# Kernel tuning notes

Measured on AMD Instinct MI355X. Metric: run time of the kernel, lower is better.

Reference implementation:

```python
import jax, jax.numpy as jnp
import numpy as np

N, E, CIN, H, HEADS, B = 50000, 800000, 16, 64, 3, 64
D0 = HEADS * H            # conv1 out (heads concatenated) = 192
D1 = D0 + CIN             # x1 dim = 208
D2 = 2 * D1               # x2 dim = 416
MLP_IN = 3 * D2           # 1248
MLP_HID = MLP_IN // 2     # 624
EPS = 1e-5


def setup_inputs() -> dict:
    key = jax.random.key(0)
    ks = jax.random.split(key, 24)
    r = lambda k, s, sc=0.05: (jax.random.normal(k, s, dtype=jnp.float32) * sc)
    inp = {
        'x': jax.random.normal(ks[0], (N, CIN), dtype=jnp.float32),
        'edge_index': jax.random.randint(ks[1], (2, E), 0, N, dtype=jnp.int32),
        'edge_attr': jax.random.normal(ks[2], (E, 4), dtype=jnp.float32),
        'batch': jnp.sort(jax.random.randint(ks[3], (N,), 0, B, dtype=jnp.int32)),
        # conv1 (GeneralConv, heads=3, concat): msg/edge/self linears -> D0
        'W_msg1': r(ks[4], (CIN, D0)), 'b_msg1': jnp.zeros((D0,), jnp.float32),
        'W_edge1': r(ks[5], (4, D0)), 'b_edge1': jnp.zeros((D0,), jnp.float32),
        'W_self1': r(ks[6], (CIN, D0)), 'b_self1': jnp.zeros((D0,), jnp.float32),
        'g1': jnp.ones((D0,), jnp.float32), 'be1': jnp.zeros((D0,), jnp.float32),
        # conv2 (GeneralConv, heads=1, in==out -> identity self)
        'W_msg2': r(ks[7], (D1, D1)), 'b_msg2': jnp.zeros((D1,), jnp.float32),
        'W_edge2': r(ks[8], (4, D1)), 'b_edge2': jnp.zeros((D1,), jnp.float32),
        'g2': jnp.ones((D1,), jnp.float32), 'be2': jnp.zeros((D1,), jnp.float32),
        # MLP head
        'W_l1': r(ks[9], (MLP_IN, MLP_HID)), 'b_l1': jnp.zeros((MLP_HID,), jnp.float32),
        'alpha': jnp.asarray(0.25, jnp.float32),  # PReLU default
        'W_l2': r(ks[10], (MLP_HID, 2)), 'b_l2': jnp.zeros((2,), jnp.float32),
    }
    return inp


def _bn(h, g, b):
    m = h.mean(axis=0)
    v = h.var(axis=0)  # biased, like torch BatchNorm training mode
    return (h - m) * jax.lax.rsqrt(v + EPS) * g + b


def reference(x, edge_index, edge_attr, batch,
              W_msg1, b_msg1, W_edge1, b_edge1, W_self1, b_self1, g1, be1,
              W_msg2, b_msg2, W_edge2, b_edge2, g2, be2,
              W_l1, b_l1, alpha, W_l2, b_l2):
    src, dst = edge_index[0], edge_index[1]
    # conv1: gather -> linear msg + edge feature -> scatter-add -> + self linear
    m1 = x[src] @ W_msg1 + b_msg1 + edge_attr @ W_edge1 + b_edge1   # [E, D0]
    h1 = jax.ops.segment_sum(m1, dst, num_segments=N) + (x @ W_self1 + b_self1)
    h1 = _bn(h1, g1, be1)
    x1 = jnp.concatenate([h1, x], axis=1)                           # [N, D1]
    # conv2 (identity self-connection since in==out)
    m2 = x1[src] @ W_msg2 + b_msg2 + edge_attr @ W_edge2 + b_edge2  # [E, D1]
    h2 = jax.ops.segment_sum(m2, dst, num_segments=N) + x1
    h2 = _bn(h2, g2, be2)
    x2 = jnp.concatenate([h2, x1], axis=1)                          # [N, D2]
    # global add / mean / max pooling by graph id
    s = jax.ops.segment_sum(x2, batch, num_segments=B)
    cnt = jax.ops.segment_sum(jnp.ones((x2.shape[0], 1), x2.dtype), batch, num_segments=B)
    mean = s / jnp.maximum(cnt, 1.0)
    mx = jax.ops.segment_max(x2, batch, num_segments=B)
    pooled = jnp.concatenate([s, mx, mean], axis=1)                 # [B, 3*D2]
    # MLP head: Linear -> Dropout(0) -> PReLU -> Linear -> log_softmax
    h = pooled @ W_l1 + b_l1
    h = jnp.where(h >= 0, h, alpha * h)
    logits = h @ W_l2 + b_l2
    return jax.nn.log_softmax(logits, axis=-1)
```

## Files before the change

### kernel.cpp

```cpp
#include <hip/hip_runtime.h>

typedef __attribute__((ext_vector_type(8))) short short8;
typedef __attribute__((ext_vector_type(4))) float f32x4;
typedef unsigned short u16;
typedef unsigned int u32;

__device__ __forceinline__ u16 f2bf(float f) {
  u32 u = __float_as_uint(f);
  u = (u + 0x7fffu + ((u >> 16) & 1u)) >> 16;
  return (u16)u;
}
__device__ __forceinline__ float bf2f(u16 v) { return __uint_as_float((u32)v << 16); }
__device__ __forceinline__ void atomAddF(float* p, float v) { unsafeAtomicAdd(p, v); }
__device__ __forceinline__ void addp(float* v, u32 p) {
  v[0] += bf2f((u16)p);
  v[1] += bf2f((u16)(p >> 16));
}

__global__ void prep_k(const float* __restrict__ Wm1, const float* __restrict__ We1,
                       const float* __restrict__ Ws1, const float* __restrict__ Wm2,
                       const float* __restrict__ Wl1, const float* __restrict__ x,
                       const int* __restrict__ batch, u16* __restrict__ Wp1,
                       u16* __restrict__ Wp2, u16* __restrict__ Wp3,
                       u16* __restrict__ xbf, int* __restrict__ gstart,
                       int* __restrict__ gend, int* __restrict__ deg,
                       float* __restrict__ bns1p, float* __restrict__ bns2p, int N, int E) {
  int tid = blockIdx.x * 256 + threadIdx.x;
  if (tid < 64 * 192) {
    int k = tid / 192, n = tid % 192;
    float v = 0.f;
    if (k < 16) v = Wm1[k * 192 + n];
    else if (k < 20) v = We1[(k - 16) * 192 + n];
    else if (k < 36) v = Ws1[(k - 20) * 192 + n];
    Wp1[((k >> 3) * 192 + n) * 8 + (k & 7)] = f2bf(v);
  }
  if (tid < 224 * 208) {
    int k = tid / 208, n = tid % 208;
    float v = (k < 208) ? Wm2[k * 208 + n] : 0.f;
    Wp2[((k >> 3) * 208 + n) * 8 + (k & 7)] = f2bf(v);
  }
  if (tid < N * 8) {
    float2 p = *(const float2*)(x + (size_t)tid * 2);
    *(u32*)(xbf + (size_t)tid * 2) = (u32)f2bf(p.x) | ((u32)f2bf(p.y) << 16);
  }
  if (tid < N) {
    int b = batch[tid];
    if (tid == 0 || batch[tid - 1] != b) gstart[b] = tid;
    if (tid == N - 1 || batch[tid + 1] != b) gend[b] = tid;
    deg[tid] = 0;
  }
  if (tid < 64 * 384) bns1p[tid] = 0.f;
  if (tid < 64 * 832) bns2p[tid] = 0.f;
  if (tid < 1248 * 624) {
    int k = tid / 624, n = tid % 624;
    Wp3[((size_t)(k >> 3) * 624 + n) * 8 + (k & 7)] = f2bf(Wl1[(size_t)k * 624 + n]);
  }
}

__global__ void count_k(const int* __restrict__ ei, int* __restrict__ deg,
                        int* __restrict__ ord, int E) {
  int e = blockIdx.x * 256 + threadIdx.x;
  if (e >= E) return;
  ord[e] = atomicAdd(&deg[ei[E + e]], 1);
}

__global__ void scanA_k(const int* __restrict__ deg, int* __restrict__ bsum, int N) {
  __shared__ int sh[256];
  int t = threadIdx.x;
  int i = blockIdx.x * 256 + t;
  sh[t] = (i < N) ? deg[i] : 0;
  __syncthreads();
  for (int off = 128; off > 0; off >>= 1) {
    if (t < off) sh[t] += sh[t + off];
    __syncthreads();
  }
  if (t == 0) bsum[blockIdx.x] = sh[0];
}

__global__ void scanC_k(const int* __restrict__ deg, const int* __restrict__ bsum,
                        int* __restrict__ rowptr, int N, int nb) {
  __shared__ int sb2[256];
  __shared__ int sh[256];
  int t = threadIdx.x;
  int bv = (t < nb) ? bsum[t] : 0;
  sb2[t] = bv;
  __syncthreads();
  for (int off = 1; off < 256; off <<= 1) {
    int u = (t >= off) ? sb2[t - off] : 0;
    __syncthreads();
    sb2[t] += u;
    __syncthreads();
  }
  int bpref = (blockIdx.x == 0) ? 0 : sb2[blockIdx.x - 1];
  int i = blockIdx.x * 256 + t;
  int d = (i < N) ? deg[i] : 0;
  sh[t] = d;
  __syncthreads();
  for (int off = 1; off < 256; off <<= 1) {
    int u = (t >= off) ? sh[t - off] : 0;
    __syncthreads();
    sh[t] += u;
    __syncthreads();
  }
  int excl = sh[t] - d + bpref;
  if (i < N) {
    rowptr[i] = excl;
    if (i == N - 1) rowptr[N] = excl + d;
  }
}

__global__ void scatter_k(const int* __restrict__ ei, const float* __restrict__ ea,
                          const int* __restrict__ ord, const int* __restrict__ rowptr,
                          int4* __restrict__ se16, int E) {
  int e = blockIdx.x * 256 + threadIdx.x;
  if (e >= E) return;
  int s = ei[e], d = ei[E + e];
  float4 w = *(const float4*)(ea + (size_t)e * 4);
  int slot = rowptr[d] + ord[e];
  int4 ent;
  ent.x = s;
  ent.y = (int)((u32)f2bf(w.x) | ((u32)f2bf(w.y) << 16));
  ent.z = (int)((u32)f2bf(w.z) | ((u32)f2bf(w.w) << 16));
  ent.w = 0;
  se16[slot] = ent;
}

__global__ void __launch_bounds__(256) gath1_k(
    const int4* __restrict__ se16, const int* __restrict__ rowptr,
    const u16* __restrict__ xbf, u16* __restrict__ acc1c, int N) {
  int tid = threadIdx.x;
  int nl = tid >> 4, q = tid & 15;
  int n = blockIdx.x * 16 + nl;
  bool nval = n < N;
  int j0 = nval ? rowptr[n] : 0;
  int j1 = nval ? rowptr[n + 1] : 0;
  float v[20];
#pragma unroll
  for (int i = 0; i < 20; ++i) v[i] = 0.f;
  {
    int j = j0 + q;
    bool a0 = j < j1, a1 = (j + 16) < j1;
    int jj0 = a0 ? j : 0;
    int jj1 = a1 ? (j + 16) : 0;
    int4 p0 = se16[jj0];
    int4 p1 = se16[jj1];
    const uint4* xs0 = (const uint4*)(xbf + (size_t)(a0 ? p0.x : 0) * 16);
    uint4 x00 = xs0[0], x01 = xs0[1];
    const uint4* xs1 = (const uint4*)(xbf + (size_t)(a1 ? p1.x : 0) * 16);
    uint4 x10 = xs1[0], x11 = xs1[1];
    if (a0) {
      addp(v + 0, x00.x); addp(v + 2, x00.y); addp(v + 4, x00.z); addp(v + 6, x00.w);
      addp(v + 8, x01.x); addp(v + 10, x01.y); addp(v + 12, x01.z); addp(v + 14, x01.w);
      addp(v + 16, (u32)p0.y); addp(v + 18, (u32)p0.z);
    }
    if (a1) {
      addp(v + 0, x10.x); addp(v + 2, x10.y); addp(v + 4, x10.z); addp(v + 6, x10.w);
      addp(v + 8, x11.x); addp(v + 10, x11.y); addp(v + 12, x11.z); addp(v + 14, x11.w);
      addp(v + 16, (u32)p1.y); addp(v + 18, (u32)p1.z);
    }
    for (j += 32; j < j1; j += 16) {
      int4 p = se16[j];
      const uint4* xs = (const uint4*)(xbf + (size_t)p.x * 16);
      uint4 x0 = xs[0], x1 = xs[1];
      addp(v + 0, x0.x); addp(v + 2, x0.y); addp(v + 4, x0.z); addp(v + 6, x0.w);
      addp(v + 8, x1.x); addp(v + 10, x1.y); addp(v + 12, x1.z); addp(v + 14, x1.w);
      addp(v + 16, (u32)p.y); addp(v + 18, (u32)p.z);
    }
  }
#pragma unroll
  for (int i = 0; i < 20; ++i) {
    v[i] += __shfl_xor(v[i], 1);
    v[i] += __shfl_xor(v[i], 2);
    v[i] += __shfl_xor(v[i], 4);
    v[i] += __shfl_xor(v[i], 8);
  }
  if (nval) {
    float degf = (float)(j1 - j0);
    int t0 = q * 2, t1 = t0 + 1;
    float f0 = (t0 < 20) ? v[t0] : ((t0 == 20) ? degf : 0.f);
    float f1 = (t1 < 20) ? v[t1] : ((t1 == 20) ? degf : 0.f);
    *(u32*)(acc1c + (size_t)n * 32 + q * 2) = (u32)f2bf(f0) | ((u32)f2bf(f1) << 16);
  }
}

__global__ void __launch_bounds__(256) gath2_k(
    const int4* __restrict__ se16, const int* __restrict__ rowptr,
    const u16* __restrict__ acc1c, u16* __restrict__ acc2, int N) {
  int tid = threadIdx.x;
  int nl = tid >> 4, q = tid & 15;
  int n = blockIdx.x * 16 + nl;
  bool nval = n < N;
  int j0 = nval ? rowptr[n] : 0;
  int j1 = nval ? rowptr[n + 1] : 0;
  float v[21];
#pragma unroll
  for (int i = 0; i < 21; ++i) v[i] = 0.f;
  {
    int j = j0 + q;
    bool a0 = j < j1, a1 = (j + 16) < j1;
    int jj0 = a0 ? j : 0;
    int jj1 = a1 ? (j + 16) : 0;
    int4 p0 = se16[jj0];
    int4 p1 = se16[jj1];
    const uint4* cr0 = (const uint4*)(acc1c + (size_t)(a0 ? p0.x : 0) * 32);
    uint4 c00 = cr0[0], c01 = cr0[1], c02 = cr0[2];
    const uint4* cr1 = (const uint4*)(acc1c + (size_t)(a1 ? p1.x : 0) * 32);
    uint4 c10 = cr1[0], c11 = cr1[1], c12 = cr1[2];
    if (a0) {
      addp(v + 0, c00.x); addp(v + 2, c00.y); addp(v + 4, c00.z); addp(v + 6, c00.w);
      addp(v + 8, c01.x); addp(v + 10, c01.y); addp(v + 12, c01.z); addp(v + 14, c01.w);
      addp(v + 16, c02.x); addp(v + 18, c02.y);
      v[20] += bf2f((u16)c02.z);
    }
    if (a1) {
      addp(v + 0, c10.x); addp(v + 2, c10.y); addp(v + 4, c10.z); addp(v + 6, c10.w);
      addp(v + 8, c11.x); addp(v + 10, c11.y); addp(v + 12, c11.z); addp(v + 14, c11.w);
      addp(v + 16, c12.x); addp(v + 18, c12.y);
      v[20] += bf2f((u16)c12.z);
    }
    for (j += 32; j < j1; j += 16) {
      int s = se16[j].x;
      const uint4* cr = (const uint4*)(acc1c + (size_t)s * 32);
      uint4 c0 = cr[0], c1 = cr[1], c2 = cr[2];
      addp(v + 0, c0.x); addp(v + 2, c0.y); addp(v + 4, c0.z); addp(v + 6, c0.w);
      addp(v + 8, c1.x); addp(v + 10, c1.y); addp(v + 12, c1.z); addp(v + 14, c1.w);
      addp(v + 16, c2.x); addp(v + 18, c2.y);
      v[20] += bf2f((u16)c2.z);
    }
  }
#pragma unroll
  for (int i = 0; i < 21; ++i) {
    v[i] += __shfl_xor(v[i], 1);
    v[i] += __shfl_xor(v[i], 2);
    v[i] += __shfl_xor(v[i], 4);
    v[i] += __shfl_xor(v[i], 8);
  }
  if (nval && q < 12) {
    int t0 = q * 2, t1 = t0 + 1;
    float f0 = (t0 < 20) ? v[t0] : ((t0 == 20) ? v[20] : 0.f);
    float f1 = (t1 < 20) ? v[t1] : ((t1 == 20) ? v[20] : 0.f);
    *(u32*)(acc2 + (size_t)n * 24 + q * 2) = (u32)f2bf(f0) | ((u32)f2bf(f1) << 16);
  }
}

__global__ void __launch_bounds__(512) mm1_k(
    const u16* __restrict__ acc1c, const u16* __restrict__ xbf,
    const u16* __restrict__ Bp, const float* __restrict__ bm1,
    const float* __restrict__ be1, const float* __restrict__ bs1,
    u16* __restrict__ h1bf, float* __restrict__ bns1p, int N) {
  __shared__ __align__(16) u16 Uls[32][72];
  __shared__ float degls[32];
  int tid = threadIdx.x;
  int nl = tid >> 4, q = tid & 15;
  int n = blockIdx.x * 32 + nl;
  bool nval = n < N;
  u32 w0 = 0, w1 = 0;
  if (nval) {
    if (q < 5) {
      w0 = *(const u32*)(acc1c + (size_t)n * 32 + q * 4);
      w1 = *(const u32*)(acc1c + (size_t)n * 32 + q * 4 + 2);
    } else if (q < 9) {
      int o = q * 4 - 20;
      w0 = *(const u32*)(xbf + (size_t)n * 16 + o);
      w1 = *(const u32*)(xbf + (size_t)n * 16 + o + 2);
    }
  }
  *(uint2*)&Uls[nl][q * 4] = make_uint2(w0, w1);
  if (q == 0) degls[nl] = nval ? bf2f(acc1c[(size_t)n * 32 + 20]) : 0.f;
  __syncthreads();
  int w = tid >> 6, lane = tid & 63, rc = lane & 15, qd = lane >> 4;
  int slice = (blockIdx.x & 63) * 384;
  for (int job = w; job < 24; job += 8) {
    int mt = job / 12, nt = job % 12;
    f32x4 acc = {0.f, 0.f, 0.f, 0.f};
#pragma unroll
    for (int kb = 0; kb < 2; ++kb) {
      short8 av = *(const short8*)&Uls[mt * 16 + rc][kb * 32 + qd * 8];
      short8 bv = *(const short8*)(Bp + (size_t)((kb * 4 + qd) * 192 + nt * 16 + rc) * 8);
      acc = __builtin_amdgcn_mfma_f32_16x16x32_bf16(av, bv, acc, 0, 0, 0);
    }
    int col = nt * 16 + rc;
    float bb = bm1[col] + be1[col], bsv = bs1[col];
    float ps = 0.f, pq = 0.f;
#pragma unroll
    for (int r = 0; r < 4; ++r) {
      int ml = mt * 16 + qd * 4 + r;
      int m = blockIdx.x * 32 + ml;
      float val = acc[r] + degls[ml] * bb + bsv;
      if (m < N) {
        h1bf[(size_t)m * 192 + col] = f2bf(val);
        ps += val;
        pq += val * val;
      }
    }
    ps += __shfl_xor(ps, 16); ps += __shfl_xor(ps, 32);
    pq += __shfl_xor(pq, 16); pq += __shfl_xor(pq, 32);
    if (qd == 0) {
      atomAddF(&bns1p[slice + col], ps);
      atomAddF(&bns1p[slice + 192 + col], pq);
    }
  }
}

__global__ void bnfin1_k(const float* __restrict__ bns1p, const float* __restrict__ g1,
                         const float* __restrict__ bta1, float Ninv,
                         float* __restrict__ aff1) {
  int c = threadIdx.x;
  if (c >= 192) return;
  float sm = 0.f, sq = 0.f;
  for (int k = 0; k < 64; ++k) {
    sm += bns1p[k * 384 + c];
    sq += bns1p[k * 384 + 192 + c];
  }
  float m1 = sm * Ninv;
  float var = sq * Ninv - m1 * m1;
  float s1 = g1[c] * rsqrtf(var + 1e-5f);
  aff1[c] = s1;
  aff1[192 + c] = bta1[c] - m1 * s1;
}

__global__ void __launch_bounds__(512) mm2_k(
    const u16* __restrict__ acc1c, const u16* __restrict__ acc2,
    const u16* __restrict__ h1bf, const u16* __restrict__ xbf,
    const u16* __restrict__ Bp1, const u16* __restrict__ Bp2,
    const float* __restrict__ bm1, const float* __restrict__ be1,
    const float* __restrict__ bs1, const float* __restrict__ aff1,
    const float* __restrict__ We2, const float* __restrict__ bm2,
    const float* __restrict__ be2, float* __restrict__ bns2p,
    u16* __restrict__ h2bf, int N) {
  __shared__ __align__(16) u16 Uls[32][72];
  __shared__ __align__(16) u16 Vls[32][232];
  __shared__ __align__(16) u16 X1ls[32][208];
  __shared__ float degls[32], sdegls[32], eals[32][4];
  int tid = threadIdx.x;
  int nl = tid >> 4, q = tid & 15;
  int n = blockIdx.x * 32 + nl;
  bool nval = n < N;
  int base = blockIdx.x * 32;

  {
    int r0 = tid / 24, c0 = tid % 24;
    int gr = base + r0;
    uint4 sg = (gr < N) ? *(const uint4*)(h1bf + (size_t)gr * 192 + c0 * 8)
                        : make_uint4(0, 0, 0, 0);
    *(uint4*)&X1ls[r0][c0 * 8] = sg;
  }
  if (tid < 256) {
    int r1 = (tid + 512) / 24, c1 = (tid + 512) % 24;
    int gr = base + r1;
    uint4 sg = (gr < N) ? *(const uint4*)(h1bf + (size_t)gr * 192 + c1 * 8)
                        : make_uint4(0, 0, 0, 0);
    *(uint4*)&X1ls[r1][c1 * 8] = sg;
  }
  if (tid < 64) {
    int gr = base + (tid >> 1);
    uint4 sg = (gr < N) ? *(const uint4*)(xbf + (size_t)gr * 16 + (tid & 1) * 8)
                        : make_uint4(0, 0, 0, 0);
    *(uint4*)&X1ls[tid >> 1][192 + (tid & 1) * 8] = sg;
  }

  {
    u32 w0 = 0, w1 = 0;
    if (nval) {
      if (q < 5) {
        w0 = *(const u32*)(acc2 + (size_t)n * 24 + q * 4);
        w1 = *(const u32*)(acc2 + (size_t)n * 24 + q * 4 + 2);
      } else if (q < 9) {
        int o = q * 4 - 20;
        w0 = *(const u32*)(acc1c + (size_t)n * 32 + o);
        w1 = *(const u32*)(acc1c + (size_t)n * 32 + o + 2);
      }
    }
    *(uint2*)&Uls[nl][q * 4] = make_uint2(w0, w1);
  }
  {
    u32 w = 0;
    if (nval && q < 8) w = *(const u32*)(acc1c + (size_t)n * 32 + q * 2);
    *(u32*)&Vls[nl][192 + q * 2] = w;
  }
  if (q == 0) sdegls[nl] = nval ? bf2f(acc2[(size_t)n * 24 + 20]) : 0.f;
  if (q == 1) degls[nl] = nval ? bf2f(acc1c[(size_t)n * 32 + 20]) : 0.f;
  if (q == 2) {
#pragma unroll
    for (int k = 0; k < 4; ++k)
      eals[nl][k] = nval ? bf2f(acc1c[(size_t)n * 32 + 16 + k]) : 0.f;
  }
  __syncthreads();
  int w = tid >> 6, lane = tid & 63, rc = lane & 15, qd = lane >> 4;
  for (int job = w; job < 24; job += 8) {
    int mt = job / 12, nt = job % 12;
    f32x4 acc = {0.f, 0.f, 0.f, 0.f};
#pragma unroll
    for (int kb = 0; kb < 2; ++kb) {
      short8 av = *(const short8*)&Uls[mt * 16 + rc][kb * 32 + qd * 8];
      short8 bv = *(const short8*)(Bp1 + (size_t)((kb * 4 + qd) * 192 + nt * 16 + rc) * 8);
      acc = __builtin_amdgcn_mfma_f32_16x16x32_bf16(av, bv, acc, 0, 0, 0);
    }
    int col = nt * 16 + rc;
    float s1 = aff1[col], t1 = aff1[192 + col];
    float bb = bm1[col] + be1[col], bsv = bs1[col];
#pragma unroll
    for (int r = 0; r < 4; ++r) {
      int ml = mt * 16 + qd * 4 + r;
      float qv = acc[r] + sdegls[ml] * bb + degls[ml] * bsv;
      Vls[ml][col] = f2bf(qv * s1 + degls[ml] * t1);
    }
  }
  __syncthreads();
  int slice = (blockIdx.x & 63) * 832;
  for (int job = w; job < 26; job += 8) {
    int mt = job / 13, nt = job % 13;
    f32x4 acc = {0.f, 0.f, 0.f, 0.f};
#pragma unroll
    for (int kb = 0; kb < 7; ++kb) {
      short8 av = *(const short8*)&Vls[mt * 16 + rc][kb * 32 + qd * 8];
      short8 bv = *(const short8*)(Bp2 + (size_t)((kb * 4 + qd) * 208 + nt * 16 + rc) * 8);
      acc = __builtin_amdgcn_mfma_f32_16x16x32_bf16(av, bv, acc, 0, 0, 0);
    }
    int col = nt * 16 + rc;
    float w0 = We2[col], w1 = We2[208 + col], w2 = We2[416 + col], w3 = We2[624 + col];
    float bb2 = bm2[col] + be2[col];
    bool c192 = col < 192;
    float s1 = c192 ? aff1[col] : 0.f;
    float t1 = c192 ? aff1[192 + col] : 0.f;
    float ps = 0.f, pq = 0.f;
#pragma unroll
    for (int r = 0; r < 4; ++r) {
      int ml = mt * 16 + qd * 4 + r;
      int m = blockIdx.x * 32 + ml;
      bool mv = m < N;
      float x1 = bf2f(X1ls[ml][col]);
      if (c192) x1 = x1 * s1 + t1;
      float val = acc[r] + eals[ml][0] * w0 + eals[ml][1] * w1 + eals[ml][2] * w2 +
                  eals[ml][3] * w3 + degls[ml] * bb2 + x1;
      if (mv) {
        h2bf[(size_t)m * 208 + col] = f2bf(val);
        ps += val;
        pq += val * val;
      }
    }
    ps += __shfl_xor(ps, 16); ps += __shfl_xor(ps, 32);
    pq += __shfl_xor(pq, 16); pq += __shfl_xor(pq, 32);
    if (qd == 0) {
      atomAddF(&bns2p[slice + col], ps);
      atomAddF(&bns2p[slice + 416 + col], pq);
    }
  }
}

__global__ void bnfin2_k(const float* __restrict__ bns2p, const float* __restrict__ aff1,
                         const float* __restrict__ g2, const float* __restrict__ bta2,
                         float Ninv, float* __restrict__ aff) {
  int f = blockIdx.x * 256 + threadIdx.x;
  if (f >= 416) return;
  float sc, sh;
  if (f < 208) {
    float sm = 0.f, sq = 0.f;
    for (int k = 0; k < 64; ++k) {
      sm += bns2p[k * 832 + f];
      sq += bns2p[k * 832 + 416 + f];
    }
    float m2 = sm * Ninv;
    float var = sq * Ninv - m2 * m2;
    sc = g2[f] * rsqrtf(var + 1e-5f);
    sh = bta2[f] - m2 * sc;
  } else if (f < 400) {
    sc = aff1[f - 208];
    sh = aff1[192 + (f - 208)];
  } else {
    sc = 1.f;
    sh = 0.f;
  }
  aff[f] = sc;
  aff[416 + f] = sh;
}

__global__ void pool_k(const u16* __restrict__ h2bf, const u16* __restrict__ h1bf,
                       const u16* __restrict__ xbf, const float* __restrict__ aff,
                       const int* __restrict__ gstart, const int* __restrict__ gend,
                       float* __restrict__ psp, float* __restrict__ pmp) {
  int b = blockIdx.x, sub = blockIdx.y;
  int t = threadIdx.x;
  if (t >= 208) return;
  int s0 = gstart[b], e0 = gend[b];
  int cnt = (s0 <= e0) ? e0 - s0 + 1 : 0;
  int per = (cnt + 15) >> 4;
  int n0 = s0 + sub * per;
  int n1 = min(n0 + per, s0 + cnt);
  int f = 2 * t;
  const u16* src;
  int stride;
  if (f < 208) { src = h2bf + f; stride = 208; }
  else if (f < 400) { src = h1bf + (f - 208); stride = 192; }
  else { src = xbf + (f - 400); stride = 16; }
  float sc0 = aff[f], sc1 = aff[f + 1];
  float sh0 = aff[416 + f], sh1 = aff[417 + f];
  float s0f = 0.f, s1f = 0.f, m0f = -3.4e38f, m1f = -3.4e38f;
  for (int n = n0; n < n1; ++n) {
    u32 p = *(const u32*)(src + (size_t)n * stride);
    float v0 = bf2f((u16)p) * sc0 + sh0;
    float v1 = bf2f((u16)(p >> 16)) * sc1 + sh1;
    s0f += v0; s1f += v1;
    m0f = fmaxf(m0f, v0); m1f = fmaxf(m1f, v1);
  }
  size_t idx = ((size_t)(b * 16 + sub)) * 416 + f;
  *(float2*)(psp + idx) = make_float2(s0f, s1f);
  *(float2*)(pmp + idx) = make_float2(m0f, m1f);
}

__global__ void pooledprep_k(const float* __restrict__ psp, const float* __restrict__ pmp,
                             const int* __restrict__ gstart, const int* __restrict__ gend,
                             u16* __restrict__ Apool) {
  int b = blockIdx.x, t = threadIdx.x;
  int cnt = gend[b] - gstart[b] + 1;
  float inv = 1.f / (float)max(cnt, 1);
  for (int f = t; f < 416; f += 256) {
    float s = 0.f, m = -3.4e38f;
    for (int k = 0; k < 16; ++k) {
      size_t idx = ((size_t)(b * 16 + k)) * 416 + f;
      s += psp[idx];
      m = fmaxf(m, pmp[idx]);
    }
    u16* row = Apool + (size_t)b * 1248;
    row[f] = f2bf(s);
    row[416 + f] = f2bf((cnt > 0) ? m : 0.f);
    row[832 + f] = f2bf(s * inv);
  }
}

__global__ void __launch_bounds__(256) mlpgemm_k(const u16* __restrict__ A,
                                                 const u16* __restrict__ Bp,
                                                 const float* __restrict__ b1,
                                                 const float* __restrict__ al,
                                                 float* __restrict__ hid) {
  __shared__ __align__(16) float part[3][64][4];
  int tid = threadIdx.x;
  int w = tid >> 6, lane = tid & 63;
  int mt = blockIdx.x, nt = blockIdx.y;
  int rc = lane & 15, qd = lane >> 4;
  f32x4 acc = {0.f, 0.f, 0.f, 0.f};
  const u16* Ap = A + (size_t)(mt * 16 + rc) * 1248 + qd * 8;
  const u16* Bq = Bp + (size_t)(qd * 624 + nt * 16 + rc) * 8;
  for (int kb = w; kb < 39; kb += 4) {
    short8 av = *(const short8*)(Ap + kb * 32);
    short8 bv = *(const short8*)(Bq + (size_t)kb * 4 * 624 * 8);
    acc = __builtin_amdgcn_mfma_f32_16x16x32_bf16(av, bv, acc, 0, 0, 0);
  }
  if (w > 0) *(f32x4*)&part[w - 1][lane][0] = acc;
  __syncthreads();
  if (w == 0) {
#pragma unroll
    for (int j = 0; j < 3; ++j) {
      f32x4 p = *(const f32x4*)&part[j][lane][0];
      acc[0] += p[0]; acc[1] += p[1]; acc[2] += p[2]; acc[3] += p[3];
    }
    int col = nt * 16 + rc;
    float bb = b1[col], alpha = al[0];
    int m0 = mt * 16 + qd * 4;
#pragma unroll
    for (int r = 0; r < 4; ++r) {
      float v = acc[r] + bb;
      hid[(size_t)(m0 + r) * 624 + col] = (v >= 0.f) ? v : alpha * v;
    }
  }
}

__global__ void head_k(const float* __restrict__ hid, const float* __restrict__ W2,
                       const float* __restrict__ b2, float* __restrict__ out) {
  int b = blockIdx.x, t = threadIdx.x;
  float p0 = 0.f, p1 = 0.f;
  for (int k = t; k < 624; k += 64) {
    float h = hid[(size_t)b * 624 + k];
    p0 += h * W2[k * 2];
    p1 += h * W2[k * 2 + 1];
  }
#pragma unroll
  for (int off = 32; off > 0; off >>= 1) {
    p0 += __shfl_down(p0, off);
    p1 += __shfl_down(p1, off);
  }
  if (t == 0) {
    float l0 = p0 + b2[0], l1 = p1 + b2[1];
    float m = fmaxf(l0, l1);
    float lse = m + logf(expf(l0 - m) + expf(l1 - m));
    out[b * 2] = l0 - lse;
    out[b * 2 + 1] = l1 - lse;
  }
}

extern "C" void kernel_launch(void* const* d_in, const int* in_sizes, int n_in,
                              void* d_out, int out_size, void* d_ws, size_t ws_size,
                              hipStream_t stream) {
  const float* x = (const float*)d_in[0];
  const int* ei = (const int*)d_in[1];
  const float* ea = (const float*)d_in[2];
  const int* batch = (const int*)d_in[3];
  const float* Wm1 = (const float*)d_in[4];
  const float* bm1 = (const float*)d_in[5];
  const float* We1 = (const float*)d_in[6];
  const float* be1 = (const float*)d_in[7];
  const float* Ws1 = (const float*)d_in[8];
  const float* bs1 = (const float*)d_in[9];
  const float* g1 = (const float*)d_in[10];
  const float* bta1 = (const float*)d_in[11];
  const float* Wm2 = (const float*)d_in[12];
  const float* bm2 = (const float*)d_in[13];
  const float* We2 = (const float*)d_in[14];
  const float* be2 = (const float*)d_in[15];
  const float* g2 = (const float*)d_in[16];
  const float* bta2 = (const float*)d_in[17];
  const float* Wl1 = (const float*)d_in[18];
  const float* bl1 = (const float*)d_in[19];
  const float* alpha = (const float*)d_in[20];
  const float* Wl2 = (const float*)d_in[21];
  const float* bl2 = (const float*)d_in[22];
  float* out = (float*)d_out;

  const int N = in_sizes[3];
  const int E = in_sizes[2] / 4;
  const int nb = (N + 255) / 256;
  const float Ninv = 1.f / (float)N;

  float* ws = (float*)d_ws;
  size_t o = 0;
  u16* acc1c = (u16*)(ws + o); o += (size_t)N * 16;
  u16* acc2 = (u16*)(ws + o);  o += (size_t)N * 12;
  u16* h2bf = (u16*)(ws + o);  o += (size_t)N * 104;
  u16* h1bf = (u16*)(ws + o);  o += (size_t)N * 96;
  u16* xbf = (u16*)(ws + o);   o += (size_t)N * 8;
  u16* Wp1 = (u16*)(ws + o);   o += 6144;
  u16* Wp2 = (u16*)(ws + o);   o += 23296;
  u16* Wp3 = (u16*)(ws + o);   o += 389376;
  u16* Apool = (u16*)(ws + o); o += 39936;
  float* hid = ws + o;    o += 64 * 624;
  float* bns1p = ws + o;  o += 64 * 384;
  float* bns2p = ws + o;  o += 64 * 832;
  float* aff1 = ws + o;   o += 384;
  float* aff = ws + o;    o += 832;
  float* psp = ws + o;    o += (size_t)64 * 16 * 416;
  float* pmp = ws + o;    o += (size_t)64 * 16 * 416;
  int* gstart = (int*)(ws + o); o += 64;
  int* gend = (int*)(ws + o);   o += 64;
  int* deg = (int*)(ws + o);    o += N;
  int* rowptr = (int*)(ws + o); o += N + 1;
  int* ord = (int*)(ws + o);    o += E;
  int* bsum = (int*)(ws + o);   o += 256;
  o = (o + 3) & ~(size_t)3;
  int4* se16 = (int4*)(ws + o); o += (size_t)4 * E;

  const int ggath = (N + 15) / 16;
  const int gmm = (N + 31) / 32;
  prep_k<<<(E + 255) / 256, 256, 0, stream>>>(Wm1, We1, Ws1, Wm2, Wl1, x, batch, Wp1, Wp2,
                                              Wp3, xbf, gstart, gend, deg, bns1p, bns2p,
                                              N, E);
  count_k<<<(E + 255) / 256, 256, 0, stream>>>(ei, deg, ord, E);
  scanA_k<<<nb, 256, 0, stream>>>(deg, bsum, N);
  scanC_k<<<nb, 256, 0, stream>>>(deg, bsum, rowptr, N, nb);
  scatter_k<<<(E + 255) / 256, 256, 0, stream>>>(ei, ea, ord, rowptr, se16, E);
  gath1_k<<<ggath, 256, 0, stream>>>(se16, rowptr, xbf, acc1c, N);
  mm1_k<<<gmm, 512, 0, stream>>>(acc1c, xbf, Wp1, bm1, be1, bs1, h1bf, bns1p, N);
  bnfin1_k<<<1, 256, 0, stream>>>(bns1p, g1, bta1, Ninv, aff1);
  gath2_k<<<ggath, 256, 0, stream>>>(se16, rowptr, acc1c, acc2, N);
  mm2_k<<<gmm, 512, 0, stream>>>(acc1c, acc2, h1bf, xbf, Wp1, Wp2, bm1, be1, bs1, aff1,
                                 We2, bm2, be2, bns2p, h2bf, N);
  bnfin2_k<<<2, 256, 0, stream>>>(bns2p, aff1, g2, bta2, Ninv, aff);
  pool_k<<<dim3(64, 16), 256, 0, stream>>>(h2bf, h1bf, xbf, aff, gstart, gend, psp, pmp);
  pooledprep_k<<<64, 256, 0, stream>>>(psp, pmp, gstart, gend, Apool);
  mlpgemm_k<<<dim3(4, 39), 256, 0, stream>>>(Apool, Wp3, bl1, alpha, hid);
  head_k<<<64, 64, 0, stream>>>(hid, Wl2, bl2, out);
}
```

Before: 292.7 us.

## Merge gather2 and mm1 into one launch, fold BN1 finalize into consumers

Combines the independent gath2 and mm1 kernels into a single launch where odd blocks do the second gather (32 nodes, 512 threads) and even blocks do the mm1 MFMA tile, so the two phases overlap on the GPU. Removes the bnfin1 launch by recomputing the BN1 affine in each mm2 block (into shared memory) and in bnfin2. This cuts two launches and their serialization gaps, at the cost of every mm2 block redundantly reducing 64x384 partial sums and the gather blocks now using larger 512-thread blocks.

```diff
diff --git a/kernel.cpp b/kernel.cpp
--- a/kernel.cpp
+++ b/kernel.cpp
@@ -183,77 +183,77 @@
   }
 }
 
-__global__ void __launch_bounds__(256) gath2_k(
+__global__ void __launch_bounds__(512) g2mm1_k(
     const int4* __restrict__ se16, const int* __restrict__ rowptr,
-    const u16* __restrict__ acc1c, u16* __restrict__ acc2, int N) {
+    const u16* __restrict__ acc1c, u16* __restrict__ acc2,
+    const u16* __restrict__ xbf, const u16* __restrict__ Bp,
+    const float* __restrict__ bm1, const float* __restrict__ be1,
+    const float* __restrict__ bs1, u16* __restrict__ h1bf,
+    float* __restrict__ bns1p, int N) {
+  __shared__ __align__(16) u16 Uls[32][72];
+  __shared__ float degls[32];
+  int bid = blockIdx.x;
+  int bid2 = bid >> 1;
   int tid = threadIdx.x;
   int nl = tid >> 4, q = tid & 15;
-  int n = blockIdx.x * 16 + nl;
+  int n = bid2 * 32 + nl;
   bool nval = n < N;
-  int j0 = nval ? rowptr[n] : 0;
-  int j1 = nval ? rowptr[n + 1] : 0;
-  float v[21];
-#pragma unroll
-  for (int i = 0; i < 21; ++i) v[i] = 0.f;
-  {
-    int j = j0 + q;
-    bool a0 = j < j1, a1 = (j + 16) < j1;
-    int jj0 = a0 ? j : 0;
-    int jj1 = a1 ? (j + 16) : 0;
-    int4 p0 = se16[jj0];
-    int4 p1 = se16[jj1];
-    const uint4* cr0 = (const uint4*)(acc1c + (size_t)(a0 ? p0.x : 0) * 32);
-    uint4 c00 = cr0[0], c01 = cr0[1], c02 = cr0[2];
-    const uint4* cr1 = (const uint4*)(acc1c + (size_t)(a1 ? p1.x : 0) * 32);
-    uint4 c10 = cr1[0], c11 = cr1[1], c12 = cr1[2];
-    if (a0) {
-      addp(v + 0, c00.x); addp(v + 2, c00.y); addp(v + 4, c00.z); addp(v + 6, c00.w);
-      addp(v + 8, c01.x); addp(v + 10, c01.y); addp(v + 12, c01.z); addp(v + 14, c01.w);
-      addp(v + 16, c02.x); addp(v + 18, c02.y);
-      v[20] += bf2f((u16)c02.z);
-    }
-    if (a1) {
-      addp(v + 0, c10.x); addp(v + 2, c10.y); addp(v + 4, c10.z); addp(v + 6, c10.w);
-      addp(v + 8, c11.x); addp(v + 10, c11.y); addp(v + 12, c11.z); addp(v + 14, c11.w);
-      addp(v + 16, c12.x); addp(v + 18, c12.y);
-      v[20] += bf2f((u16)c12.z);
-    }
-    for (j += 32; j < j1; j += 16) {
-      int s = se16[j].x;
-      const uint4* cr = (const uint4*)(acc1c + (size_t)s * 32);
-      uint4 c0 = cr[0], c1 = cr[1], c2 = cr[2];
-      addp(v + 0, c0.x); addp(v + 2, c0.y); addp(v + 4, c0.z); addp(v + 6, c0.w);
-      addp(v + 8, c1.x); addp(v + 10, c1.y); addp(v + 12, c1.z); addp(v + 14, c1.w);
-      addp(v + 16, c2.x); addp(v + 18, c2.y);
-      v[20] += bf2f((u16)c2.z);
-    }
-  }
-#pragma unroll
-  for (int i = 0; i < 21; ++i) {
-    v[i] += __shfl_xor(v[i], 1);
-    v[i] += __shfl_xor(v[i], 2);
-    v[i] += __shfl_xor(v[i], 4);
-    v[i] += __shfl_xor(v[i], 8);
-  }
-  if (nval && q < 12) {
-    int t0 = q * 2, t1 = t0 + 1;
-    float f0 = (t0 < 20) ? v[t0] : ((t0 == 20) ? v[20] : 0.f);
-    float f1 = (t1 < 20) ? v[t1] : ((t1 == 20) ? v[20] : 0.f);
-    *(u32*)(acc2 + (size_t)n * 24 + q * 2) = (u32)f2bf(f0) | ((u32)f2bf(f1) << 16);
-  }
-}
-
-__global__ void __launch_bounds__(512) mm1_k(
-    const u16* __restrict__ acc1c, const u16* __restrict__ xbf,
-    const u16* __restrict__ Bp, const float* __restrict__ bm1,
-    const float* __restrict__ be1, const float* __restrict__ bs1,
-    u16* __restrict__ h1bf, float* __restrict__ bns1p, int N) {
-  __shared__ __align__(16) u16 Uls[32][72];
-  __shared__ float degls[32];
-  int tid = threadIdx.x;
-  int nl = tid >> 4, q = tid & 15;
-  int n = blockIdx.x * 32 + nl;
-  bool nval = n < N;
+
+  if (bid & 1) {
+    int j0 = nval ? rowptr[n] : 0;
+    int j1 = nval ? rowptr[n + 1] : 0;
+    float v[21];
+#pragma unroll
+    for (int i = 0; i < 21; ++i) v[i] = 0.f;
+    {
+      int j = j0 + q;
+      bool a0 = j < j1, a1 = (j + 16) < j1;
+      int jj0 = a0 ? j : 0;
+      int jj1 = a1 ? (j + 16) : 0;
+      int4 p0 = se16[jj0];
+      int4 p1 = se16[jj1];
+      const uint4* cr0 = (const uint4*)(acc1c + (size_t)(a0 ? p0.x : 0) * 32);
+      uint4 c00 = cr0[0], c01 = cr0[1], c02 = cr0[2];
+      const uint4* cr1 = (const uint4*)(acc1c + (size_t)(a1 ? p1.x : 0) * 32);
+      uint4 c10 = cr1[0], c11 = cr1[1], c12 = cr1[2];
+      if (a0) {
+        addp(v + 0, c00.x); addp(v + 2, c00.y); addp(v + 4, c00.z); addp(v + 6, c00.w);
+        addp(v + 8, c01.x); addp(v + 10, c01.y); addp(v + 12, c01.z); addp(v + 14, c01.w);
+        addp(v + 16, c02.x); addp(v + 18, c02.y);
+        v[20] += bf2f((u16)c02.z);
+      }
+      if (a1) {
+        addp(v + 0, c10.x); addp(v + 2, c10.y); addp(v + 4, c10.z); addp(v + 6, c10.w);
+        addp(v + 8, c11.x); addp(v + 10, c11.y); addp(v + 12, c11.z); addp(v + 14, c11.w);
+        addp(v + 16, c12.x); addp(v + 18, c12.y);
+        v[20] += bf2f((u16)c12.z);
+      }
+      for (j += 32; j < j1; j += 16) {
+        int s = se16[j].x;
+        const uint4* cr = (const uint4*)(acc1c + (size_t)s * 32);
+        uint4 c0 = cr[0], c1 = cr[1], c2 = cr[2];
+        addp(v + 0, c0.x); addp(v + 2, c0.y); addp(v + 4, c0.z); addp(v + 6, c0.w);
+        addp(v + 8, c1.x); addp(v + 10, c1.y); addp(v + 12, c1.z); addp(v + 14, c1.w);
+        addp(v + 16, c2.x); addp(v + 18, c2.y);
+        v[20] += bf2f((u16)c2.z);
+      }
+    }
+#pragma unroll
+    for (int i = 0; i < 21; ++i) {
+      v[i] += __shfl_xor(v[i], 1);
+      v[i] += __shfl_xor(v[i], 2);
+      v[i] += __shfl_xor(v[i], 4);
+      v[i] += __shfl_xor(v[i], 8);
+    }
+    if (nval && q < 12) {
+      int t0 = q * 2, t1 = t0 + 1;
+      float f0 = (t0 < 20) ? v[t0] : ((t0 == 20) ? v[20] : 0.f);
+      float f1 = (t1 < 20) ? v[t1] : ((t1 == 20) ? v[20] : 0.f);
+      *(u32*)(acc2 + (size_t)n * 24 + q * 2) = (u32)f2bf(f0) | ((u32)f2bf(f1) << 16);
+    }
+    return;
+  }
+
   u32 w0 = 0, w1 = 0;
   if (nval) {
     if (q < 5) {
@@ -269,7 +269,7 @@
   if (q == 0) degls[nl] = nval ? bf2f(acc1c[(size_t)n * 32 + 20]) : 0.f;
   __syncthreads();
   int w = tid >> 6, lane = tid & 63, rc = lane & 15, qd = lane >> 4;
-  int slice = (blockIdx.x & 63) * 384;
+  int slice = (bid2 & 63) * 384;
   for (int job = w; job < 24; job += 8) {
     int mt = job / 12, nt = job % 12;
     f32x4 acc = {0.f, 0.f, 0.f, 0.f};
@@ -285,7 +285,7 @@
 #pragma unroll
     for (int r = 0; r < 4; ++r) {
       int ml = mt * 16 + qd * 4 + r;
-      int m = blockIdx.x * 32 + ml;
+      int m = bid2 * 32 + ml;
       float val = acc[r] + degls[ml] * bb + bsv;
       if (m < N) {
         h1bf[(size_t)m * 192 + col] = f2bf(val);
@@ -302,29 +302,13 @@
   }
 }
 
-__global__ void bnfin1_k(const float* __restrict__ bns1p, const float* __restrict__ g1,
-                         const float* __restrict__ bta1, float Ninv,
-                         float* __restrict__ aff1) {
-  int c = threadIdx.x;
-  if (c >= 192) return;
-  float sm = 0.f, sq = 0.f;
-  for (int k = 0; k < 64; ++k) {
-    sm += bns1p[k * 384 + c];
-    sq += bns1p[k * 384 + 192 + c];
-  }
-  float m1 = sm * Ninv;
-  float var = sq * Ninv - m1 * m1;
-  float s1 = g1[c] * rsqrtf(var + 1e-5f);
-  aff1[c] = s1;
-  aff1[192 + c] = bta1[c] - m1 * s1;
-}
-
 __global__ void __launch_bounds__(512) mm2_k(
     const u16* __restrict__ acc1c, const u16* __restrict__ acc2,
     const u16* __restrict__ h1bf, const u16* __restrict__ xbf,
     const u16* __restrict__ Bp1, const u16* __restrict__ Bp2,
     const float* __restrict__ bm1, const float* __restrict__ be1,
-    const float* __restrict__ bs1, const float* __restrict__ aff1,
+    const float* __restrict__ bs1, const float* __restrict__ bns1p,
+    const float* __restrict__ g1, const float* __restrict__ bta1, float Ninv,
     const float* __restrict__ We2, const float* __restrict__ bm2,
     const float* __restrict__ be2, float* __restrict__ bns2p,
     u16* __restrict__ h2bf, int N) {
@@ -332,6 +316,7 @@
   __shared__ __align__(16) u16 Vls[32][232];
   __shared__ __align__(16) u16 X1ls[32][208];
   __shared__ float degls[32], sdegls[32], eals[32][4];
+  __shared__ float aff1ls[384];
   int tid = threadIdx.x;
   int nl = tid >> 4, q = tid & 15;
   int n = blockIdx.x * 32 + nl;
@@ -357,6 +342,19 @@
     uint4 sg = (gr < N) ? *(const uint4*)(xbf + (size_t)gr * 16 + (tid & 1) * 8)
                         : make_uint4(0, 0, 0, 0);
     *(uint4*)&X1ls[tid >> 1][192 + (tid & 1) * 8] = sg;
+  }
+
+  if (tid < 192) {
+    float sm = 0.f, sq = 0.f;
+    for (int k = 0; k < 64; ++k) {
+      sm += bns1p[k * 384 + tid];
+      sq += bns1p[k * 384 + 192 + tid];
+    }
+    float m1 = sm * Ninv;
+    float var = sq * Ninv - m1 * m1;
+    float s1 = g1[tid] * rsqrtf(var + 1e-5f);
+    aff1ls[tid] = s1;
+    aff1ls[192 + tid] = bta1[tid] - m1 * s1;
   }
 
   {
@@ -397,7 +395,7 @@
       acc = __builtin_amdgcn_mfma_f32_16x16x32_bf16(av, bv, acc, 0, 0, 0);
     }
     int col = nt * 16 + rc;
-    float s1 = aff1[col], t1 = aff1[192 + col];
+    float s1 = aff1ls[col], t1 = aff1ls[192 + col];
     float bb = bm1[col] + be1[col], bsv = bs1[col];
 #pragma unroll
     for (int r = 0; r < 4; ++r) {
@@ -421,8 +419,8 @@
     float w0 = We2[col], w1 = We2[208 + col], w2 = We2[416 + col], w3 = We2[624 + col];
     float bb2 = bm2[col] + be2[col];
     bool c192 = col < 192;
-    float s1 = c192 ? aff1[col] : 0.f;
-    float t1 = c192 ? aff1[192 + col] : 0.f;
+    float s1 = c192 ? aff1ls[col] : 0.f;
+    float t1 = c192 ? aff1ls[192 + col] : 0.f;
     float ps = 0.f, pq = 0.f;
 #pragma unroll
     for (int r = 0; r < 4; ++r) {
@@ -448,7 +446,8 @@
   }
 }
 
-__global__ void bnfin2_k(const float* __restrict__ bns2p, const float* __restrict__ aff1,
+__global__ void bnfin2_k(const float* __restrict__ bns2p, const float* __restrict__ bns1p,
+                         const float* __restrict__ g1, const float* __restrict__ bta1,
                          const float* __restrict__ g2, const float* __restrict__ bta2,
                          float Ninv, float* __restrict__ aff) {
   int f = blockIdx.x * 256 + threadIdx.x;
@@ -465,8 +464,16 @@
     sc = g2[f] * rsqrtf(var + 1e-5f);
     sh = bta2[f] - m2 * sc;
   } else if (f < 400) {
-    sc = aff1[f - 208];
-    sh = aff1[192 + (f - 208)];
+    int c = f - 208;
+    float sm = 0.f, sq = 0.f;
+    for (int k = 0; k < 64; ++k) {
+      sm += bns1p[k * 384 + c];
+      sq += bns1p[k * 384 + 192 + c];
+    }
+    float m1 = sm * Ninv;
+    float var = sq * Ninv - m1 * m1;
+    sc = g1[c] * rsqrtf(var + 1e-5f);
+    sh = bta1[c] - m1 * sc;
   } else {
     sc = 1.f;
     sh = 0.f;
@@ -635,7 +642,6 @@
   float* hid = ws + o;    o += 64 * 624;
   float* bns1p = ws + o;  o += 64 * 384;
   float* bns2p = ws + o;  o += 64 * 832;
-  float* aff1 = ws + o;   o += 384;
   float* aff = ws + o;    o += 832;
   float* psp = ws + o;    o += (size_t)64 * 16 * 416;
   float* pmp = ws + o;    o += (size_t)64 * 16 * 416;
@@ -658,12 +664,11 @@
   scanC_k<<<nb, 256, 0, stream>>>(deg, bsum, rowptr, N, nb);
   scatter_k<<<(E + 255) / 256, 256, 0, stream>>>(ei, ea, ord, rowptr, se16, E);
   gath1_k<<<ggath, 256, 0, stream>>>(se16, rowptr, xbf, acc1c, N);
-  mm1_k<<<gmm, 512, 0, stream>>>(acc1c, xbf, Wp1, bm1, be1, bs1, h1bf, bns1p, N);
-  bnfin1_k<<<1, 256, 0, stream>>>(bns1p, g1, bta1, Ninv, aff1);
-  gath2_k<<<ggath, 256, 0, stream>>>(se16, rowptr, acc1c, acc2, N);
-  mm2_k<<<gmm, 512, 0, stream>>>(acc1c, acc2, h1bf, xbf, Wp1, Wp2, bm1, be1, bs1, aff1,
-                                 We2, bm2, be2, bns2p, h2bf, N);
-  bnfin2_k<<<2, 256, 0, stream>>>(bns2p, aff1, g2, bta2, Ninv, aff);
+  g2mm1_k<<<2 * gmm, 512, 0, stream>>>(se16, rowptr, acc1c, acc2, xbf, Wp1, bm1, be1,
+                                       bs1, h1bf, bns1p, N);
+  mm2_k<<<gmm, 512, 0, stream>>>(acc1c, acc2, h1bf, xbf, Wp1, Wp2, bm1, be1, bs1, bns1p,
+                                 g1, bta1, Ninv, We2, bm2, be2, bns2p, h2bf, N);
+  bnfin2_k<<<2, 256, 0, stream>>>(bns2p, bns1p, g1, bta1, g2, bta2, Ninv, aff);
   pool_k<<<dim3(64, 16), 256, 0, stream>>>(h2bf, h1bf, xbf, aff, gstart, gend, psp, pmp);
   pooledprep_k<<<64, 256, 0, stream>>>(psp, pmp, gstart, gend, Apool);
   mlpgemm_k<<<dim3(4, 39), 256, 0, stream>>>(Apool, Wp3, bl1, alpha, hid);
```

After: 294.6 us. About the same (+0.7%).
